# Kernel tuning notes

Hardware: AMD Instinct MI355X
Metric: run time of the kernel (lower is better)

Reference implementation:

```python
import jax, jax.numpy as jnp
import numpy as np

B, L, D, DFF, DLLM, E, TOPK = 16, 512, 768, 3072, 4096, 8, 2
EPS_GATE = 1e-9
LN_EPS = 1e-5


def _layernorm(x, gamma, beta):
    mu = jnp.mean(x, axis=-1, keepdims=True)
    var = jnp.var(x, axis=-1, keepdims=True)
    return (x - mu) * jax.lax.rsqrt(var + LN_EPS) * gamma + beta


def _mlp_block(x, w1, b1, w2, b2, gamma, beta):
    # MLPBlock: Linear -> GELU -> Linear -> LayerNorm(residual). Dropout is identity in eval.
    h = jax.nn.gelu(x @ w1 + b1)
    o = h @ w2 + b2
    return _layernorm(o + x, gamma, beta)


def setup_inputs() -> dict:
    key = jax.random.key(0)
    ks = jax.random.split(key, 24)
    sd = lambda fan_in: 1.0 / np.sqrt(fan_in)
    inp = {
        'cycle_curve_data': jax.random.normal(ks[0], (B, L, D), jnp.float32),
        'cycle_numbers': jax.random.uniform(ks[1], (B, 1), jnp.float32) * 1000.0,
        'DKP_embeddings': jax.random.normal(ks[2], (B, DLLM), jnp.float32),
        # Gate (PatternRouter_two): fuses LLM embedding + cycle number -> expert logits
        'gate_We': jax.random.normal(ks[3], (DLLM, DFF), jnp.float32) * sd(DLLM),
        'gate_Wc': jax.random.normal(ks[4], (1, DFF), jnp.float32),
        'gate_b': jnp.zeros((DFF,), jnp.float32),
        'gate_Wo': jax.random.normal(ks[5], (DFF, E), jnp.float32) * sd(DFF),
        'gate_bo': jnp.zeros((E,), jnp.float32),
        # Stacked expert params [E, ...]
        'e_w1': jax.random.normal(ks[6], (E, D, DFF), jnp.float32) * sd(D),
        'e_b1': jnp.zeros((E, DFF), jnp.float32),
        'e_w2': jax.random.normal(ks[7], (E, DFF, D), jnp.float32) * sd(DFF),
        'e_b2': jnp.zeros((E, D), jnp.float32),
        'e_gamma': jnp.ones((E, D), jnp.float32),
        'e_beta': jnp.zeros((E, D), jnp.float32),
        # General expert
        'g_w1': jax.random.normal(ks[8], (D, DFF), jnp.float32) * sd(D),
        'g_b1': jnp.zeros((DFF,), jnp.float32),
        'g_w2': jax.random.normal(ks[9], (DFF, D), jnp.float32) * sd(DFF),
        'g_b2': jnp.zeros((D,), jnp.float32),
        'g_gamma': jnp.ones((D,), jnp.float32),
        'g_beta': jnp.zeros((D,), jnp.float32),
    }
    return inp


def reference(cycle_curve_data, cycle_numbers, DKP_embeddings,
              gate_We, gate_Wc, gate_b, gate_Wo, gate_bo,
              e_w1, e_b1, e_w2, e_b2, e_gamma, e_beta,
              g_w1, g_b1, g_w2, g_b2, g_gamma, g_beta):
    # --- Router: clean logits (eval mode: no noise) ---
    h = jax.nn.relu(DKP_embeddings @ gate_We + cycle_numbers @ gate_Wc + gate_b)
    logits = h @ gate_Wo + gate_bo                         # [B, E]
    _, idx = jax.lax.top_k(logits, TOPK)                   # [B, TOPK]
    probs = jax.nn.softmax(logits, axis=1)
    mask = jnp.zeros_like(probs).at[jnp.arange(B)[:, None], idx].set(1.0)
    gated = probs * mask
    gated = gated / (jnp.sum(gated, axis=1, keepdims=True) + EPS_GATE)  # [B, E]

    # --- Experts: dense compute, zero gates zero out non-routed experts ---
    x = cycle_curve_data
    combined = jnp.zeros_like(x)
    for e in range(E):  # small fixed expert count
        out_e = _mlp_block(x, e_w1[e], e_b1[e], e_w2[e], e_b2[e], e_gamma[e], e_beta[e])
        combined = combined + gated[:, e, None, None] * out_e

    general = _mlp_block(x, g_w1, g_b1, g_w2, g_b2, g_gamma, g_beta)
    final_out = general + combined.astype(jnp.bfloat16)  # matches .to(torch.bfloat16) cast before add
    return final_out
```

## Files before the change

### kernel.cpp

```cpp
#include <hip/hip_runtime.h>
#include <cstdint>

#define B_    16
#define L_    512
#define D_    768
#define DFF_  3072
#define DLLM_ 4096
#define E_    8

typedef unsigned short ushort_t;
typedef __attribute__((ext_vector_type(4))) float accfrag_t;
typedef __attribute__((ext_vector_type(8))) short bfrag_t;

typedef __attribute__((address_space(3))) uint32_t lds_u32;
typedef __attribute__((address_space(1))) uint32_t glb_u32;

__device__ inline void gload16(const void* g, void* l) {
  __builtin_amdgcn_global_load_lds((const glb_u32*)(uintptr_t)g,
                                   (lds_u32*)(uint32_t)(uintptr_t)l, 16, 0, 0);
}

__device__ inline ushort_t f2bf(float f) {
  uint32_t u = __float_as_uint(f);
  return (ushort_t)((u + 0x7FFFu + ((u >> 16) & 1u)) >> 16);
}
__device__ inline float bf2f(ushort_t v) { return __uint_as_float(((uint32_t)v) << 16); }

#define MFMA16(a, b, c) __builtin_amdgcn_mfma_f32_16x16x32_bf16(a, b, c, 0, 0, 0)

template <int KT>
__device__ __forceinline__ void gemm_body(const char* gA, const char* gB,
                                          char* sm, accfrag_t acc[4][6]) {
  const int tid = threadIdx.x;
  const int lane = tid & 63;
  const int w = tid >> 6, wm = w >> 1, wn = w & 1;
  const int LDB = KT * 128;

  const int R0 = tid >> 3;
  const int swz = (((tid & 7) ^ (R0 & 7)) << 4);
  const char* srcA = gA + (size_t)R0 * LDB + swz;
  const char* srcB = gB + (size_t)R0 * LDB + swz;
  const int dl = tid * 16;

  const int l15 = lane & 15, l7 = lane & 7, lhi = lane >> 4;
  const int a0 = (wm * 64 + l15) * 128 + ((lhi ^ l7) << 4);
  const int a1 = (wm * 64 + l15) * 128 + (((4 + lhi) ^ l7) << 4);
  const int b0 = 16384 + (wn * 96 + l15) * 128 + ((lhi ^ l7) << 4);
  const int b1 = 16384 + (wn * 96 + l15) * 128 + (((4 + lhi) ^ l7) << 4);

#pragma unroll 1
  for (int t = 0; t < KT; ++t) {
    const size_t ko = (size_t)t * 128;
#pragma unroll
    for (int j = 0; j < 4; ++j)
      gload16(srcA + (size_t)j * 32 * LDB + ko, sm + j * 4096 + dl);
#pragma unroll
    for (int j = 0; j < 6; ++j)
      gload16(srcB + (size_t)j * 32 * LDB + ko, sm + 16384 + j * 4096 + dl);
    __syncthreads();
    {
      bfrag_t af[4], bf[6];
#pragma unroll
      for (int nf = 0; nf < 6; ++nf) bf[nf] = *(const bfrag_t*)(sm + b0 + nf * 2048);
#pragma unroll
      for (int mf = 0; mf < 4; ++mf) af[mf] = *(const bfrag_t*)(sm + a0 + mf * 2048);
      __builtin_amdgcn_s_setprio(1);
#pragma unroll
      for (int mf = 0; mf < 4; ++mf)
#pragma unroll
        for (int nf = 0; nf < 6; ++nf)
          acc[mf][nf] = MFMA16(af[mf], bf[nf], acc[mf][nf]);
      __builtin_amdgcn_s_setprio(0);
    }
    __builtin_amdgcn_sched_barrier(0);
    {
      bfrag_t af[4], bf[6];
#pragma unroll
      for (int nf = 0; nf < 6; ++nf) bf[nf] = *(const bfrag_t*)(sm + b1 + nf * 2048);
#pragma unroll
      for (int mf = 0; mf < 4; ++mf) af[mf] = *(const bfrag_t*)(sm + a1 + mf * 2048);
      __builtin_amdgcn_s_setprio(1);
#pragma unroll
      for (int mf = 0; mf < 4; ++mf)
#pragma unroll
        for (int nf = 0; nf < 6; ++nf)
          acc[mf][nf] = MFMA16(af[mf], bf[nf], acc[mf][nf]);
      __builtin_amdgcn_s_setprio(0);
    }
    __syncthreads();
  }
}

__device__ inline void job_tile(int f, int tilesPerJob, int jp_count,
                                int& jobIdx, int& t) {
  if ((jp_count & 7) == 0) {
    const int xcd = f & 7, slot = f >> 3;
    jobIdx = xcd + 8 * (slot / tilesPerJob);
    t = slot % tilesPerJob;
  } else {
    jobIdx = f / tilesPerJob;
    t = f % tilesPerJob;
  }
}

__global__ __launch_bounds__(256, 3)
void gemm1_k(const ushort_t* __restrict__ xb, const ushort_t* __restrict__ w1t,
             const float* __restrict__ e_b1, const float* __restrict__ g_b1,
             const int* __restrict__ tidx, ushort_t* __restrict__ h_out,
             int job0, int jp_count) {
  __shared__ char sm[40960];
  int jp, t;
  job_tile(blockIdx.x, 64, jp_count, jp, t);
  const int mt = t >> 4, nt = t & 15;
  const int job = job0 + jp;
  const int b = job / 3, s = job - b * 3;
  const int e = (s < 2) ? tidx[b * 2 + s] : E_;
  const char* gA = (const char*)(xb + ((size_t)b * L_ + mt * 128) * D_);
  const char* gB = (const char*)(w1t + ((size_t)e * DFF_ + nt * 192) * D_);
  accfrag_t acc[4][6] = {};
  gemm_body<12>(gA, gB, sm, acc);

  const float* b1 = (s < 2) ? (e_b1 + (size_t)e * DFF_) : g_b1;
  const int lane = threadIdx.x & 63, w = threadIdx.x >> 6;
  const int wm = w >> 1, wn = w & 1;
  const int row0 = mt * 128 + wm * 64 + ((lane >> 4) << 2);
  const int col0 = nt * 192 + wn * 96 + (lane & 15);
  float bias[6];
#pragma unroll
  for (int nf = 0; nf < 6; ++nf) bias[nf] = b1[col0 + nf * 16];
  ushort_t* hp = h_out + (size_t)jp * L_ * DFF_ + (size_t)row0 * DFF_ + col0;
#pragma unroll
  for (int mf = 0; mf < 4; ++mf)
#pragma unroll
    for (int r = 0; r < 4; ++r) {
      ushort_t* hr_ = hp + (size_t)(mf * 16 + r) * DFF_;
#pragma unroll
      for (int nf = 0; nf < 6; ++nf) {
        float v = acc[mf][nf][r] + bias[nf];
        float u = 0.7978845608028654f * (v + 0.044715f * v * v * v);
        float th = 1.0f - 2.0f / (1.0f + __expf(2.0f * u));
        hr_[nf * 16] = f2bf(0.5f * v * (1.0f + th));
      }
    }
}

__global__ __launch_bounds__(256, 3)
void gemm2_k(const ushort_t* __restrict__ h_in, const ushort_t* __restrict__ w2t,
             const float* __restrict__ e_b2, const float* __restrict__ g_b2,
             const float* __restrict__ x_f, const int* __restrict__ tidx,
             ushort_t* __restrict__ slot_o, float* __restrict__ outp,
             int job0, int jp_count) {
  __shared__ char sm[40960];
  int jp, t;
  job_tile(blockIdx.x, 16, jp_count, jp, t);
  const int mt = t >> 2, nt = t & 3;
  const int job = job0 + jp;
  const int b = job / 3, s = job - b * 3;
  const int e = (s < 2) ? tidx[b * 2 + s] : E_;
  const char* gA = (const char*)(h_in + ((size_t)jp * L_ + mt * 128) * DFF_);
  const char* gB = (const char*)(w2t + ((size_t)e * D_ + nt * 192) * DFF_);
  accfrag_t acc[4][6] = {};
  gemm_body<48>(gA, gB, sm, acc);

  const float* b2 = (s < 2) ? (e_b2 + (size_t)e * D_) : g_b2;
  const int lane = threadIdx.x & 63, w = threadIdx.x >> 6;
  const int wm = w >> 1, wn = w & 1;
  const int row0 = mt * 128 + wm * 64 + ((lane >> 4) << 2);
  const int col0 = nt * 192 + wn * 96 + (lane & 15);
  float bias[6];
#pragma unroll
  for (int nf = 0; nf < 6; ++nf) bias[nf] = b2[col0 + nf * 16];
#pragma unroll
  for (int mf = 0; mf < 4; ++mf)
#pragma unroll
    for (int r = 0; r < 4; ++r) {
      const int row = row0 + mf * 16 + r;
      const float* xr = x_f + ((size_t)b * L_ + row) * D_ + col0;
#pragma unroll
      for (int nf = 0; nf < 6; ++nf) {
        float v = acc[mf][nf][r] + bias[nf] + xr[nf * 16];
        if (s < 2)
          slot_o[(((size_t)b * 2 + s) * L_ + row) * D_ + col0 + nf * 16] = f2bf(v);
        else
          outp[((size_t)b * L_ + row) * D_ + col0 + nf * 16] = v;
      }
    }
}

__global__ __launch_bounds__(256)
void transpose_cvt_k(const float* __restrict__ srcE, const float* __restrict__ srcG,
                     ushort_t* __restrict__ dst, int R, int C) {
  const int z = blockIdx.z;
  const float* src = (z < 8) ? (srcE + (size_t)z * R * C) : srcG;
  ushort_t* out = dst + (size_t)z * R * C;
  __shared__ float tile[64][65];
  const int c0 = blockIdx.x * 64, r0 = blockIdx.y * 64;
  const int t = threadIdx.x;
  const int rr = t >> 4, cc = (t & 15) * 4;
#pragma unroll
  for (int i = 0; i < 4; ++i) {
    const float4 v = *(const float4*)(src + (size_t)(r0 + rr + i * 16) * C + c0 + cc);
    tile[rr + i * 16][cc] = v.x; tile[rr + i * 16][cc + 1] = v.y;
    tile[rr + i * 16][cc + 2] = v.z; tile[rr + i * 16][cc + 3] = v.w;
  }
  __syncthreads();
  const int c = t >> 2, r8 = (t & 3) * 16;
#pragma unroll
  for (int j = 0; j < 2; ++j) {
    ushort_t u[8];
#pragma unroll
    for (int k = 0; k < 8; ++k) u[k] = f2bf(tile[r8 + j * 8 + k][c]);
    *(uint4*)(out + (size_t)(c0 + c) * R + r0 + r8 + j * 8) = *(const uint4*)u;
  }
}

__global__ void cvt_x_k(const float* __restrict__ in, ushort_t* __restrict__ out) {
  const int i = (blockIdx.x * 256 + threadIdx.x) * 4;
  const float4 v = *(const float4*)(in + i);
  uint2 u;
  u.x = (uint32_t)f2bf(v.x) | ((uint32_t)f2bf(v.y) << 16);
  u.y = (uint32_t)f2bf(v.z) | ((uint32_t)f2bf(v.w) << 16);
  *(uint2*)(out + i) = u;
}

__global__ __launch_bounds__(256)
void router_partial_k(const float* __restrict__ emb, const float* __restrict__ We,
                      float* __restrict__ rp) {
  const int nt = blockIdx.x, kb = blockIdx.y;
  const int tid = threadIdx.x;
  __shared__ float semb[B_][256];
  const int k0 = kb * 256;
#pragma unroll
  for (int r = 0; r < B_; ++r) semb[r][tid] = emb[(size_t)r * DLLM_ + k0 + tid];
  __syncthreads();
  const int f = nt * 256 + tid;
  float acc[B_] = {};
  for (int k = 0; k < 256; ++k) {
    const float wv = We[(size_t)(k0 + k) * DFF_ + f];
#pragma unroll
    for (int j = 0; j < B_; ++j) acc[j] += semb[j][k] * wv;
  }
#pragma unroll
  for (int j = 0; j < B_; ++j)
    rp[((size_t)kb * B_ + j) * DFF_ + f] = acc[j];
}

__global__ __launch_bounds__(256)
void router_final_k(const float* __restrict__ rp, const float* __restrict__ cyc,
                    const float* __restrict__ Wc, const float* __restrict__ gb,
                    const float* __restrict__ Wo, const float* __restrict__ bo,
                    int* __restrict__ tidx, float* __restrict__ gates) {
  const int b = blockIdx.x, tid = threadIdx.x;
  const float cycb = cyc[b];
  float acc[E_] = {};
#pragma unroll
  for (int fi = 0; fi < 12; ++fi) {
    const int f = tid + fi * 256;
    float sv = 0.0f;
#pragma unroll
    for (int kb = 0; kb < 16; ++kb)
      sv += rp[((size_t)kb * B_ + b) * DFF_ + f];
    sv += cycb * Wc[f] + gb[f];
    sv = fmaxf(sv, 0.0f);
#pragma unroll
    for (int o = 0; o < E_; ++o) acc[o] += sv * Wo[(size_t)f * E_ + o];
  }
  __shared__ float lred[E_][4];
#pragma unroll
  for (int o = 0; o < E_; ++o) {
    float v = acc[o];
#pragma unroll
    for (int off = 32; off > 0; off >>= 1) v += __shfl_down(v, off, 64);
    if ((tid & 63) == 0) lred[o][tid >> 6] = v;
  }
  __syncthreads();
  if (tid == 0) {
    float lg[E_];
    float mx = -1e30f;
    for (int o = 0; o < E_; ++o) {
      lg[o] = lred[o][0] + lred[o][1] + lred[o][2] + lred[o][3] + bo[o];
      mx = fmaxf(mx, lg[o]);
    }
    int i1 = 0;
    for (int o = 1; o < E_; ++o) if (lg[o] > lg[i1]) i1 = o;
    int i2 = (i1 == 0) ? 1 : 0;
    for (int o = 0; o < E_; ++o) if (o != i1 && lg[o] > lg[i2]) i2 = o;
    float p[E_], sum = 0.0f;
    for (int o = 0; o < E_; ++o) { p[o] = __expf(lg[o] - mx); sum += p[o]; }
    const float p1 = p[i1] / sum, p2 = p[i2] / sum;
    const float den = p1 + p2 + 1e-9f;
    tidx[b * 2] = i1; tidx[b * 2 + 1] = i2;
    gates[b * 2] = p1 / den; gates[b * 2 + 1] = p2 / den;
  }
}

__global__ __launch_bounds__(256)
void final_ln_k(float* __restrict__ outp, const ushort_t* __restrict__ so,
                const float* __restrict__ gates, const int* __restrict__ tidx,
                const float* __restrict__ e_gam, const float* __restrict__ e_bet,
                const float* __restrict__ g_gam, const float* __restrict__ g_bet) {
  const int row = blockIdx.x;
  const int b = row >> 9, l = row & 511;
  const int tid = threadIdx.x;
  __shared__ float red4[4];
  float* gr = outp + (size_t)row * D_;
  const ushort_t* s0 = so + (((size_t)b * 2 + 0) * L_ + l) * D_;
  const ushort_t* s1 = so + (((size_t)b * 2 + 1) * L_ + l) * D_;
  float a0[3], a1[3], a2[3];
#pragma unroll
  for (int j = 0; j < 3; ++j) {
    const int d = tid + j * 256;
    a0[j] = gr[d];
    a1[j] = bf2f(s0[d]);
    a2[j] = bf2f(s1[d]);
  }
  auto bsum = [&](float v) -> float {
#pragma unroll
    for (int o = 32; o > 0; o >>= 1) v += __shfl_down(v, o, 64);
    if ((tid & 63) == 0) red4[tid >> 6] = v;
    __syncthreads();
    const float r = red4[0] + red4[1] + red4[2] + red4[3];
    __syncthreads();
    return r;
  };
  const float sg = bsum(a0[0] + a0[1] + a0[2]);
  const float qg = bsum(a0[0] * a0[0] + a0[1] * a0[1] + a0[2] * a0[2]);
  const float s0s = bsum(a1[0] + a1[1] + a1[2]);
  const float q0s = bsum(a1[0] * a1[0] + a1[1] * a1[1] + a1[2] * a1[2]);
  const float s1s = bsum(a2[0] + a2[1] + a2[2]);
  const float q1s = bsum(a2[0] * a2[0] + a2[1] * a2[1] + a2[2] * a2[2]);
  const float inv = 1.0f / 768.0f;
  const float mug = sg * inv, rg = rsqrtf(qg * inv - mug * mug + 1e-5f);
  const float mu0 = s0s * inv, r0 = rsqrtf(q0s * inv - mu0 * mu0 + 1e-5f);
  const float mu1 = s1s * inv, r1 = rsqrtf(q1s * inv - mu1 * mu1 + 1e-5f);
  const int e0 = tidx[b * 2], e1 = tidx[b * 2 + 1];
  const float g0 = gates[b * 2], g1 = gates[b * 2 + 1];
#pragma unroll
  for (int j = 0; j < 3; ++j) {
    const int d = tid + j * 256;
    const float lng = (a0[j] - mug) * rg * g_gam[d] + g_bet[d];
    const float ln0 = (a1[j] - mu0) * r0 * e_gam[(size_t)e0 * D_ + d] + e_bet[(size_t)e0 * D_ + d];
    const float ln1 = (a2[j] - mu1) * r1 * e_gam[(size_t)e1 * D_ + d] + e_bet[(size_t)e1 * D_ + d];
    const float comb = g0 * ln0 + g1 * ln1;
    gr[d] = lng + bf2f(f2bf(comb));
  }
}

extern "C" void kernel_launch(void* const* d_in, const int* in_sizes, int n_in,
                              void* d_out, int out_size, void* d_ws, size_t ws_size,
                              hipStream_t stream) {
  const float* x_f  = (const float*)d_in[0];
  const float* cyc  = (const float*)d_in[1];
  const float* emb  = (const float*)d_in[2];
  const float* We   = (const float*)d_in[3];
  const float* Wc   = (const float*)d_in[4];
  const float* gb   = (const float*)d_in[5];
  const float* Wo   = (const float*)d_in[6];
  const float* bo   = (const float*)d_in[7];
  const float* e_w1 = (const float*)d_in[8];
  const float* e_b1 = (const float*)d_in[9];
  const float* e_w2 = (const float*)d_in[10];
  const float* e_b2 = (const float*)d_in[11];
  const float* e_gam = (const float*)d_in[12];
  const float* e_bet = (const float*)d_in[13];
  const float* g_w1 = (const float*)d_in[14];
  const float* g_b1 = (const float*)d_in[15];
  const float* g_w2 = (const float*)d_in[16];
  const float* g_b2 = (const float*)d_in[17];
  const float* g_gam = (const float*)d_in[18];
  const float* g_bet = (const float*)d_in[19];
  float* outp = (float*)d_out;
  char* ws = (char*)d_ws;

  size_t off = 0;
  auto alloc = [&](size_t bytes) { size_t o = off; off = (off + bytes + 255) & ~(size_t)255; return o; };
  const size_t o_idx  = alloc(32 * 4);
  const size_t o_gate = alloc(32 * 4);
  const size_t o_rp   = alloc((size_t)16 * B_ * DFF_ * 4);
  const size_t o_xb   = alloc((size_t)B_ * L_ * D_ * 2);
  const size_t o_w1t  = alloc((size_t)9 * DFF_ * D_ * 2);
  const size_t o_w2t  = alloc((size_t)9 * D_ * DFF_ * 2);
  const size_t o_so   = alloc((size_t)B_ * 2 * L_ * D_ * 2);
  const size_t o_h    = off;

  int JP = 1;
  const int divs[10] = {48, 24, 16, 12, 8, 6, 4, 3, 2, 1};
  for (int k = 0; k < 10; ++k) {
    if (o_h + (size_t)divs[k] * L_ * DFF_ * 2 <= ws_size) { JP = divs[k]; break; }
  }

  ushort_t* xb    = (ushort_t*)(ws + o_xb);
  ushort_t* w1t   = (ushort_t*)(ws + o_w1t);
  ushort_t* w2t   = (ushort_t*)(ws + o_w2t);
  ushort_t* so    = (ushort_t*)(ws + o_so);
  ushort_t* h_ws  = (ushort_t*)(ws + o_h);
  int*      tidx  = (int*)(ws + o_idx);
  float*    gates = (float*)(ws + o_gate);
  float*    rp    = (float*)(ws + o_rp);

  cvt_x_k<<<dim3((B_ * L_ * D_) / 1024), dim3(256), 0, stream>>>(x_f, xb);
  transpose_cvt_k<<<dim3(DFF_ / 64, D_ / 64, 9), dim3(256), 0, stream>>>(e_w1, g_w1, w1t, D_, DFF_);
  transpose_cvt_k<<<dim3(D_ / 64, DFF_ / 64, 9), dim3(256), 0, stream>>>(e_w2, g_w2, w2t, DFF_, D_);
  router_partial_k<<<dim3(12, 16), dim3(256), 0, stream>>>(emb, We, rp);
  router_final_k<<<dim3(16), dim3(256), 0, stream>>>(rp, cyc, Wc, gb, Wo, bo, tidx, gates);

  const int passes = 48 / JP;
  for (int p = 0; p < passes; ++p) {
    gemm1_k<<<dim3(64 * JP), dim3(256), 0, stream>>>(xb, w1t, e_b1, g_b1, tidx, h_ws, p * JP, JP);
    gemm2_k<<<dim3(16 * JP), dim3(256), 0, stream>>>(h_ws, w2t, e_b2, g_b2, x_f, tidx, so, outp, p * JP, JP);
  }
  final_ln_k<<<dim3(B_ * L_), dim3(256), 0, stream>>>(outp, so, gates, tidx,
                                                      e_gam, e_bet, g_gam, g_bet);
}
```

Measured before the change: 437.3 us.

## Rewrite gemm1 as 256x256 tile, 8-wave double-buffered pipelined kernel

Replaces the gemm1 main loop with a 512-thread kernel that computes 256x256 output tiles and double-buffers K-slices in 128KB of dynamic LDS. Global-to-LDS loads for the next K step are issued between quadrant MFMA phases and gated with explicit vmcnt waits and barriers. This is meant to hide load latency and raise arithmetic intensity per LDS byte. In exchange occupancy drops to one block per CU and many more barriers are executed. gemm2 keeps the old body.

Measured after the change: 464.4 us. 1.06x slower.

```diff
diff --git a/kernel.cpp b/kernel.cpp
--- a/kernel.cpp
+++ b/kernel.cpp
@@ -28,12 +28,16 @@
 
 #define MFMA16(a, b, c) __builtin_amdgcn_mfma_f32_16x16x32_bf16(a, b, c, 0, 0, 0)
 
+#define GATE4 asm volatile("s_waitcnt vmcnt(4)" ::: "memory");
+#define BAR_  { asm volatile("" ::: "memory"); __builtin_amdgcn_s_barrier(); \
+                asm volatile("" ::: "memory"); }
+
 template <int KT>
-__device__ __forceinline__ void gemm_body(const char* gA, const char* gB,
-                                          char* sm, accfrag_t acc[4][6]) {
+__device__ __forceinline__ void gemm8p(const char* gA, const char* gB,
+                                       char* sm, accfrag_t acc[2][2][4][2]) {
   const int tid = threadIdx.x;
   const int lane = tid & 63;
-  const int w = tid >> 6, wm = w >> 1, wn = w & 1;
+  const int w = tid >> 6, wm = (w >> 2) & 1, wn = w & 3;
   const int LDB = KT * 128;
 
   const int R0 = tid >> 3;
@@ -43,51 +47,100 @@
   const int dl = tid * 16;
 
   const int l15 = lane & 15, l7 = lane & 7, lhi = lane >> 4;
-  const int a0 = (wm * 64 + l15) * 128 + ((lhi ^ l7) << 4);
-  const int a1 = (wm * 64 + l15) * 128 + (((4 + lhi) ^ l7) << 4);
-  const int b0 = 16384 + (wn * 96 + l15) * 128 + ((lhi ^ l7) << 4);
-  const int b1 = 16384 + (wn * 96 + l15) * 128 + (((4 + lhi) ^ l7) << 4);
+  const int c0 = ((lhi ^ l7) << 4), c1 = (((4 + lhi) ^ l7) << 4);
+  const int aB = (wm * 64 + l15) * 128;
+  const int bB = 32768 + (wn * 32 + l15) * 128;
+
+  auto STG_A = [&](int T, int H) {
+    char* d = sm + ((T & 1) << 16) + (H << 14) + dl;
+    const char* s = srcA + (size_t)(H * 128) * LDB + (size_t)T * 128;
+    gload16(s, d);
+    gload16(s + (size_t)64 * LDB, d + 8192);
+  };
+  auto STG_B = [&](int T, int H) {
+    char* d = sm + ((T & 1) << 16) + 32768 + (H << 14) + dl;
+    const char* s = srcB + (size_t)(H * 128) * LDB + (size_t)T * 128;
+    gload16(s, d);
+    gload16(s + (size_t)64 * LDB, d + 8192);
+  };
+
+  bfrag_t a0f[4][2], a1f[4][2], bf0[2][2], bf1[2][2];
+
+  STG_A(0, 0); STG_B(0, 0); STG_A(0, 1); STG_B(0, 1);
+  GATE4 BAR_
 
 #pragma unroll 1
   for (int t = 0; t < KT; ++t) {
-    const size_t ko = (size_t)t * 128;
-#pragma unroll
-    for (int j = 0; j < 4; ++j)
-      gload16(srcA + (size_t)j * 32 * LDB + ko, sm + j * 4096 + dl);
-#pragma unroll
-    for (int j = 0; j < 6; ++j)
-      gload16(srcB + (size_t)j * 32 * LDB + ko, sm + 16384 + j * 4096 + dl);
-    __syncthreads();
-    {
-      bfrag_t af[4], bf[6];
-#pragma unroll
-      for (int nf = 0; nf < 6; ++nf) bf[nf] = *(const bfrag_t*)(sm + b0 + nf * 2048);
-#pragma unroll
-      for (int mf = 0; mf < 4; ++mf) af[mf] = *(const bfrag_t*)(sm + a0 + mf * 2048);
-      __builtin_amdgcn_s_setprio(1);
-#pragma unroll
-      for (int mf = 0; mf < 4; ++mf)
-#pragma unroll
-        for (int nf = 0; nf < 6; ++nf)
-          acc[mf][nf] = MFMA16(af[mf], bf[nf], acc[mf][nf]);
-      __builtin_amdgcn_s_setprio(0);
-    }
-    __builtin_amdgcn_sched_barrier(0);
-    {
-      bfrag_t af[4], bf[6];
-#pragma unroll
-      for (int nf = 0; nf < 6; ++nf) bf[nf] = *(const bfrag_t*)(sm + b1 + nf * 2048);
-#pragma unroll
-      for (int mf = 0; mf < 4; ++mf) af[mf] = *(const bfrag_t*)(sm + a1 + mf * 2048);
-      __builtin_amdgcn_s_setprio(1);
-#pragma unroll
-      for (int mf = 0; mf < 4; ++mf)
-#pragma unroll
-        for (int nf = 0; nf < 6; ++nf)
-          acc[mf][nf] = MFMA16(af[mf], bf[nf], acc[mf][nf]);
-      __builtin_amdgcn_s_setprio(0);
-    }
-    __syncthreads();
+    const char* bu = sm + ((t & 1) << 16);
+    const bool st = (t + 1 < KT);
+#pragma unroll
+    for (int mf = 0; mf < 4; ++mf) {
+      a0f[mf][0] = *(const bfrag_t*)(bu + aB + mf * 2048 + c0);
+      a0f[mf][1] = *(const bfrag_t*)(bu + aB + mf * 2048 + c1);
+    }
+#pragma unroll
+    for (int nf = 0; nf < 2; ++nf) {
+      bf0[nf][0] = *(const bfrag_t*)(bu + bB + nf * 2048 + c0);
+      bf0[nf][1] = *(const bfrag_t*)(bu + bB + nf * 2048 + c1);
+    }
+    if (st) STG_A(t + 1, 0);
+    GATE4 BAR_
+    __builtin_amdgcn_s_setprio(1);
+#pragma unroll
+    for (int mf = 0; mf < 4; ++mf)
+#pragma unroll
+      for (int nf = 0; nf < 2; ++nf) {
+        acc[0][0][mf][nf] = MFMA16(a0f[mf][0], bf0[nf][0], acc[0][0][mf][nf]);
+        acc[0][0][mf][nf] = MFMA16(a0f[mf][1], bf0[nf][1], acc[0][0][mf][nf]);
+      }
+    __builtin_amdgcn_s_setprio(0);
+    BAR_
+#pragma unroll
+    for (int mf = 0; mf < 4; ++mf) {
+      a1f[mf][0] = *(const bfrag_t*)(bu + 16384 + aB + mf * 2048 + c0);
+      a1f[mf][1] = *(const bfrag_t*)(bu + 16384 + aB + mf * 2048 + c1);
+    }
+    if (st) STG_B(t + 1, 0);
+    GATE4 BAR_
+    __builtin_amdgcn_s_setprio(1);
+#pragma unroll
+    for (int mf = 0; mf < 4; ++mf)
+#pragma unroll
+      for (int nf = 0; nf < 2; ++nf) {
+        acc[1][0][mf][nf] = MFMA16(a1f[mf][0], bf0[nf][0], acc[1][0][mf][nf]);
+        acc[1][0][mf][nf] = MFMA16(a1f[mf][1], bf0[nf][1], acc[1][0][mf][nf]);
+      }
+    __builtin_amdgcn_s_setprio(0);
+    BAR_
+#pragma unroll
+    for (int nf = 0; nf < 2; ++nf) {
+      bf1[nf][0] = *(const bfrag_t*)(bu + 16384 + bB + nf * 2048 + c0);
+      bf1[nf][1] = *(const bfrag_t*)(bu + 16384 + bB + nf * 2048 + c1);
+    }
+    if (st) STG_A(t + 1, 1);
+    BAR_
+    __builtin_amdgcn_s_setprio(1);
+#pragma unroll
+    for (int mf = 0; mf < 4; ++mf)
+#pragma unroll
+      for (int nf = 0; nf < 2; ++nf) {
+        acc[1][1][mf][nf] = MFMA16(a1f[mf][0], bf1[nf][0], acc[1][1][mf][nf]);
+        acc[1][1][mf][nf] = MFMA16(a1f[mf][1], bf1[nf][1], acc[1][1][mf][nf]);
+      }
+    __builtin_amdgcn_s_setprio(0);
+    BAR_
+    if (st) STG_B(t + 1, 1);
+    GATE4 BAR_
+    __builtin_amdgcn_s_setprio(1);
+#pragma unroll
+    for (int mf = 0; mf < 4; ++mf)
+#pragma unroll
+      for (int nf = 0; nf < 2; ++nf) {
+        acc[0][1][mf][nf] = MFMA16(a0f[mf][0], bf1[nf][0], acc[0][1][mf][nf]);
+        acc[0][1][mf][nf] = MFMA16(a0f[mf][1], bf1[nf][1], acc[0][1][mf][nf]);
+      }
+    __builtin_amdgcn_s_setprio(0);
+    BAR_
   }
 }
 
@@ -103,45 +156,110 @@
   }
 }
 
-__global__ __launch_bounds__(256, 3)
+__global__ __launch_bounds__(512, 1)
 void gemm1_k(const ushort_t* __restrict__ xb, const ushort_t* __restrict__ w1t,
              const float* __restrict__ e_b1, const float* __restrict__ g_b1,
              const int* __restrict__ tidx, ushort_t* __restrict__ h_out,
              int job0, int jp_count) {
-  __shared__ char sm[40960];
+  extern __shared__ char sm[];
   int jp, t;
-  job_tile(blockIdx.x, 64, jp_count, jp, t);
-  const int mt = t >> 4, nt = t & 15;
+  job_tile(blockIdx.x, 24, jp_count, jp, t);
+  const int mt = t / 12, nt = t % 12;
   const int job = job0 + jp;
   const int b = job / 3, s = job - b * 3;
   const int e = (s < 2) ? tidx[b * 2 + s] : E_;
-  const char* gA = (const char*)(xb + ((size_t)b * L_ + mt * 128) * D_);
-  const char* gB = (const char*)(w1t + ((size_t)e * DFF_ + nt * 192) * D_);
-  accfrag_t acc[4][6] = {};
-  gemm_body<12>(gA, gB, sm, acc);
+  const char* gA = (const char*)(xb + ((size_t)b * L_ + mt * 256) * D_);
+  const char* gB = (const char*)(w1t + ((size_t)e * DFF_ + nt * 256) * D_);
+  accfrag_t acc[2][2][4][2] = {};
+  gemm8p<12>(gA, gB, sm, acc);
 
   const float* b1 = (s < 2) ? (e_b1 + (size_t)e * DFF_) : g_b1;
   const int lane = threadIdx.x & 63, w = threadIdx.x >> 6;
-  const int wm = w >> 1, wn = w & 1;
-  const int row0 = mt * 128 + wm * 64 + ((lane >> 4) << 2);
-  const int col0 = nt * 192 + wn * 96 + (lane & 15);
-  float bias[6];
-#pragma unroll
-  for (int nf = 0; nf < 6; ++nf) bias[nf] = b1[col0 + nf * 16];
-  ushort_t* hp = h_out + (size_t)jp * L_ * DFF_ + (size_t)row0 * DFF_ + col0;
-#pragma unroll
-  for (int mf = 0; mf < 4; ++mf)
-#pragma unroll
-    for (int r = 0; r < 4; ++r) {
-      ushort_t* hr_ = hp + (size_t)(mf * 16 + r) * DFF_;
-#pragma unroll
-      for (int nf = 0; nf < 6; ++nf) {
-        float v = acc[mf][nf][r] + bias[nf];
-        float u = 0.7978845608028654f * (v + 0.044715f * v * v * v);
-        float th = 1.0f - 2.0f / (1.0f + __expf(2.0f * u));
-        hr_[nf * 16] = f2bf(0.5f * v * (1.0f + th));
+  const int wm = (w >> 2) & 1, wn = w & 3;
+  ushort_t* hj = h_out + (size_t)jp * L_ * DFF_;
+#pragma unroll
+  for (int mq = 0; mq < 2; ++mq)
+#pragma unroll
+    for (int nq = 0; nq < 2; ++nq)
+#pragma unroll
+      for (int nf = 0; nf < 2; ++nf) {
+        const int col = nt * 256 + nq * 128 + wn * 32 + nf * 16 + (lane & 15);
+        const float bias = b1[col];
+#pragma unroll
+        for (int mf = 0; mf < 4; ++mf)
+#pragma unroll
+          for (int r = 0; r < 4; ++r) {
+            const int row = mt * 256 + mq * 128 + wm * 64 + mf * 16 +
+                            ((lane >> 4) << 2) + r;
+            float v = acc[mq][nq][mf][nf][r] + bias;
+            float u = 0.7978845608028654f * (v + 0.044715f * v * v * v);
+            float th = 1.0f - 2.0f / (1.0f + __expf(2.0f * u));
+            hj[(size_t)row * DFF_ + col] = f2bf(0.5f * v * (1.0f + th));
+          }
       }
-    }
+}
+
+template <int KT>
+__device__ __forceinline__ void gemm_body(const char* gA, const char* gB,
+                                          char* sm, accfrag_t acc[4][6]) {
+  const int tid = threadIdx.x;
+  const int lane = tid & 63;
+  const int w = tid >> 6, wm = w >> 1, wn = w & 1;
+  const int LDB = KT * 128;
+
+  const int R0 = tid >> 3;
+  const int swz = (((tid & 7) ^ (R0 & 7)) << 4);
+  const char* srcA = gA + (size_t)R0 * LDB + swz;
+  const char* srcB = gB + (size_t)R0 * LDB + swz;
+  const int dl = tid * 16;
+
+  const int l15 = lane & 15, l7 = lane & 7, lhi = lane >> 4;
+  const int a0 = (wm * 64 + l15) * 128 + ((lhi ^ l7) << 4);
+  const int a1 = (wm * 64 + l15) * 128 + (((4 + lhi) ^ l7) << 4);
+  const int b0 = 16384 + (wn * 96 + l15) * 128 + ((lhi ^ l7) << 4);
+  const int b1 = 16384 + (wn * 96 + l15) * 128 + (((4 + lhi) ^ l7) << 4);
+
+#pragma unroll 1
+  for (int t = 0; t < KT; ++t) {
+    const size_t ko = (size_t)t * 128;
+#pragma unroll
+    for (int j = 0; j < 4; ++j)
+      gload16(srcA + (size_t)j * 32 * LDB + ko, sm + j * 4096 + dl);
+#pragma unroll
+    for (int j = 0; j < 6; ++j)
+      gload16(srcB + (size_t)j * 32 * LDB + ko, sm + 16384 + j * 4096 + dl);
+    __syncthreads();
+    {
+      bfrag_t af[4], bf[6];
+#pragma unroll
+      for (int nf = 0; nf < 6; ++nf) bf[nf] = *(const bfrag_t*)(sm + b0 + nf * 2048);
+#pragma unroll
+      for (int mf = 0; mf < 4; ++mf) af[mf] = *(const bfrag_t*)(sm + a0 + mf * 2048);
+      __builtin_amdgcn_s_setprio(1);
+#pragma unroll
+      for (int mf = 0; mf < 4; ++mf)
+#pragma unroll
+        for (int nf = 0; nf < 6; ++nf)
+          acc[mf][nf] = MFMA16(af[mf], bf[nf], acc[mf][nf]);
+      __builtin_amdgcn_s_setprio(0);
+    }
+    __builtin_amdgcn_sched_barrier(0);
+    {
+      bfrag_t af[4], bf[6];
+#pragma unroll
+      for (int nf = 0; nf < 6; ++nf) bf[nf] = *(const bfrag_t*)(sm + b1 + nf * 2048);
+#pragma unroll
+      for (int mf = 0; mf < 4; ++mf) af[mf] = *(const bfrag_t*)(sm + a1 + mf * 2048);
+      __builtin_amdgcn_s_setprio(1);
+#pragma unroll
+      for (int mf = 0; mf < 4; ++mf)
+#pragma unroll
+        for (int nf = 0; nf < 6; ++nf)
+          acc[mf][nf] = MFMA16(af[mf], bf[nf], acc[mf][nf]);
+      __builtin_amdgcn_s_setprio(0);
+    }
+    __syncthreads();
+  }
 }
 
 __global__ __launch_bounds__(256, 3)
@@ -398,6 +516,8 @@
   float*    gates = (float*)(ws + o_gate);
   float*    rp    = (float*)(ws + o_rp);
 
+  hipFuncSetAttribute((const void*)gemm1_k, hipFuncAttributeMaxDynamicSharedMemorySize, 131072);
+
   cvt_x_k<<<dim3((B_ * L_ * D_) / 1024), dim3(256), 0, stream>>>(x_f, xb);
   transpose_cvt_k<<<dim3(DFF_ / 64, D_ / 64, 9), dim3(256), 0, stream>>>(e_w1, g_w1, w1t, D_, DFF_);
   transpose_cvt_k<<<dim3(D_ / 64, DFF_ / 64, 9), dim3(256), 0, stream>>>(e_w2, g_w2, w2t, DFF_, D_);
@@ -406,7 +526,7 @@
 
   const int passes = 48 / JP;
   for (int p = 0; p < passes; ++p) {
-    gemm1_k<<<dim3(64 * JP), dim3(256), 0, stream>>>(xb, w1t, e_b1, g_b1, tidx, h_ws, p * JP, JP);
+    gemm1_k<<<dim3(24 * JP), dim3(512), 131072, stream>>>(xb, w1t, e_b1, g_b1, tidx, h_ws, p * JP, JP);
     gemm2_k<<<dim3(16 * JP), dim3(256), 0, stream>>>(h_ws, w2t, e_b2, g_b2, x_f, tidx, so, outp, p * JP, JP);
   }
   final_ln_k<<<dim3(B_ * L_), dim3(256), 0, stream>>>(outp, so, gates, tidx,
```
